# Performance work log

Measured on AMD Instinct MI355X. Metric: run time of the kernel, lower is better.

## Reference

```python
import jax, jax.numpy as jnp
import numpy as np

B, T, N = 4, 512, 16
D, H = 256, 8
CTS, CN, CE = 6, 4, 3
TSE, AUXE = 192, 64  # TSE + AUXE == D
DK = D // H


def pe_table(L, d):
    # sinusoidal positional encoding (annotated-transformer style)
    pos = jnp.arange(L, dtype=jnp.float32)[:, None]
    div = jnp.exp(jnp.arange(0, d, 2, dtype=jnp.float32) * (-jnp.log(jnp.float32(10000.0)) / d))
    pe = jnp.zeros((L, d), dtype=jnp.float32)
    pe = pe.at[:, 0::2].set(jnp.sin(pos * div)).at[:, 1::2].set(jnp.cos(pos * div))
    return pe


def setup_inputs() -> dict:
    key = jax.random.key(0)
    ks = jax.random.split(key, 32)
    s = 0.02
    inp = {
        'x': jax.random.normal(ks[0], (B, T, D), jnp.float32),
        'masked_data': jax.random.normal(ks[1], (B, N, CTS, T), jnp.float32),
        'node_aux': jax.random.normal(ks[2], (B, N, CN, T), jnp.float32),
        'edge_aux': jax.random.normal(ks[3], (B, N, CE, T), jnp.float32),
        'attention_mask': jax.random.randint(ks[4], (B, T, N * T), 0, 2, jnp.int32),
        # ts branch
        'W_ts1': jax.random.normal(ks[5], (CTS, TSE)) * s, 'b_ts1': jnp.zeros((TSE,)),
        'W_ts2': jax.random.normal(ks[6], (TSE, TSE)) * s, 'b_ts2': jnp.zeros((TSE,)),
        # node aux branch
        'W_a1': jax.random.normal(ks[7], (CN, AUXE)) * s, 'b_a1': jnp.zeros((AUXE,)),
        'W_a2': jax.random.normal(ks[8], (AUXE, AUXE)) * s, 'b_a2': jnp.zeros((AUXE,)),
        # edge branch
        'W_e1': jax.random.normal(ks[9], (CE, D)) * s, 'b_e1': jnp.zeros((D,)),
        'W_e2': jax.random.normal(ks[10], (D, D)) * s, 'b_e2': jnp.zeros((D,)),
        # multi-head cross-attention
        'Wq': jax.random.normal(ks[11], (D, D)) * s, 'bq': jnp.zeros((D,)),
        'Wk': jax.random.normal(ks[12], (D, D)) * s, 'bk': jnp.zeros((D,)),
        'Wv': jax.random.normal(ks[13], (D, D)) * s, 'bv': jnp.zeros((D,)),
        'Wo': jax.random.normal(ks[14], (D, D)) * s, 'bo': jnp.zeros((D,)),
        # sublayer layernorm
        'ln_g': jnp.ones((D,)), 'ln_b': jnp.zeros((D,)),
    }
    return inp


def reference(x, masked_data, node_aux, edge_aux, attention_mask,
              W_ts1, b_ts1, W_ts2, b_ts2, W_a1, b_a1, W_a2, b_a2,
              W_e1, b_e1, W_e2, b_e2, Wq, bq, Wk, bk, Wv, bv, Wo, bo,
              ln_g, ln_b):
    pe = pe_table(T, D)  # [T, D]
    xq = x + pe[None]  # pe applied to query sequence (dropout=identity in eval)

    # per-neighbor ts MLP: transpose [B,N,C,T] -> [B,N,T,C], two Linears with ReLU between
    ts = jax.nn.relu(jnp.einsum('bnct,ce->bnte', masked_data, W_ts1) + b_ts1)
    ts = ts @ W_ts2 + b_ts2  # [B,N,T,TSE]
    aux = jax.nn.relu(jnp.einsum('bnct,ce->bnte', node_aux, W_a1) + b_a1)
    aux = aux @ W_a2 + b_a2  # [B,N,T,AUXE]
    nbr = jnp.concatenate([ts, aux], axis=-1)  # [B,N,T,D]

    edge = jax.nn.relu(jnp.einsum('bnct,cd->bntd', edge_aux, W_e1) + b_e1)
    edge = edge @ W_e2 + b_e2  # [B,N,T,D]

    # PE applied per neighbor (positions restart each neighbor), then concat over kv seq
    keys = (nbr * edge + pe[None, None]).reshape(B, N * T, D)
    vals = (nbr + pe[None, None]).reshape(B, N * T, D)

    # SublayerConnection: xq + attn(LayerNorm(xq), keys, vals, mask)
    mu = xq.mean(-1, keepdims=True)
    var = ((xq - mu) ** 2).mean(-1, keepdims=True)
    xn = (xq - mu) / jnp.sqrt(var + 1e-6) * ln_g + ln_b

    q = (xn @ Wq + bq).reshape(B, T, H, DK).transpose(0, 2, 1, 3)        # [B,H,T,DK]
    k = (keys @ Wk + bk).reshape(B, N * T, H, DK).transpose(0, 2, 1, 3)  # [B,H,NT,DK]
    v = (vals @ Wv + bv).reshape(B, N * T, H, DK).transpose(0, 2, 1, 3)

    scores = jnp.einsum('bhqd,bhkd->bhqk', q, k) / jnp.sqrt(jnp.float32(DK))
    scores = jnp.where(attention_mask[:, None, :, :] == 0, jnp.float32(-1e9), scores)
    attn = jax.nn.softmax(scores, axis=-1)
    ctx = jnp.einsum('bhqk,bhkd->bhqd', attn, v).transpose(0, 2, 1, 3).reshape(B, T, D)
    out = ctx @ Wo + bo
    return xq + out
```

## Files before the change

kernel.cpp:

```cpp
#include <hip/hip_runtime.h>
#include <hip/hip_bf16.h>

#define B_ 4
#define T_ 512
#define N_ 16
#define D_ 256
#define H_ 8
#define DK_ 32
#define NT_ (N_ * T_)
#define CTS_ 6
#define CN_ 4
#define CE_ 3
#define TSE_ 192
#define AUXE_ 64
#define SPLIT_ 8
#define KWORDS_ (NT_ / 64)

#define QSCALE_ 0.2550689747f

#define HTS_S 204
#define HAUX_S 76
#define HED_S 268
#define SK_S 268

typedef unsigned long long ull;
typedef unsigned int uint;
typedef __bf16 bf16x8 __attribute__((ext_vector_type(8)));
typedef float f32x4 __attribute__((ext_vector_type(4)));
typedef float f32x16 __attribute__((ext_vector_type(16)));

__global__ __launch_bounds__(256) void pe_kernel(float* pe) {
    int t = blockIdx.x;
    int d = threadIdx.x;
    int j = d >> 1;
    float div = expf((float)(2 * j) * (-9.210340371976184f / 256.0f));
    float a = (float)t * div;
    pe[t * D_ + d] = (d & 1) ? cosf(a) : sinf(a);
}

__global__ __launch_bounds__(256) void maskbits_kernel(const int* __restrict__ mask,
                                                       ull* __restrict__ bitsT) {
    int row = blockIdx.x;
    int b = row >> 9, t = row & (T_ - 1);
    const int* mrow = mask + (size_t)row * NT_;
    int lane = threadIdx.x & 63, wave = threadIdx.x >> 6;
    for (int it = 0; it < NT_ / 256; ++it) {
        int k = it * 256 + wave * 64 + lane;
        ull bal = __ballot(mrow[k] != 0);
        if (lane == 0) bitsT[((size_t)b * KWORDS_ + (k >> 6)) * T_ + t] = bal;
    }
}

__global__ __launch_bounds__(256) void wprep_kernel(
    const float* __restrict__ W_ts1, const float* __restrict__ W_a1,
    const float* __restrict__ W_e1, const float* __restrict__ W_ts2,
    const float* __restrict__ W_a2, const float* __restrict__ W_e2,
    const float* __restrict__ Wk, const float* __restrict__ Wv,
    const float* __restrict__ Wq, const float* __restrict__ Wo,
    __bf16* __restrict__ ts1P, __bf16* __restrict__ a1P, __bf16* __restrict__ e1P,
    __bf16* __restrict__ ts2T, __bf16* __restrict__ a2T, __bf16* __restrict__ e2T,
    __bf16* __restrict__ WkT, __bf16* __restrict__ WvT,
    __bf16* __restrict__ WqT, __bf16* __restrict__ WoT) {
    int i = blockIdx.x * 256 + threadIdx.x;
    if (i < 6144) { int col = i >> 5, k = i & 31;
        ts1P[i] = (__bf16)(k < 6 ? W_ts1[k * TSE_ + col] : 0.f); return; }
    i -= 6144;
    if (i < 2048) { int col = i >> 5, k = i & 31;
        a1P[i] = (__bf16)((k >= 6 && k < 10) ? W_a1[(k - 6) * AUXE_ + col] : 0.f); return; }
    i -= 2048;
    if (i < 8192) { int col = i >> 5, k = i & 31;
        e1P[i] = (__bf16)((k >= 10 && k < 13) ? W_e1[(k - 10) * D_ + col] : 0.f); return; }
    i -= 8192;
    if (i < 36864) {
        int tile = i >> 9, lr = (i >> 5) & 15, kk = i & 31;
        int ct = tile / 6, ks = tile % 6;
        ts2T[i] = (__bf16)W_ts2[(ks * 32 + kk) * TSE_ + ct * 16 + lr]; return; }
    i -= 36864;
    if (i < 4096) {
        int tile = i >> 9, lr = (i >> 5) & 15, kk = i & 31;
        int ct = tile / 2, ks = tile % 2;
        a2T[i] = (__bf16)W_a2[(ks * 32 + kk) * AUXE_ + ct * 16 + lr]; return; }
    i -= 4096;
    if (i < 65536) {
        int tile = i >> 9, lr = (i >> 5) & 15, kk = i & 31;
        int ct = tile >> 3, ks = tile & 7;
        e2T[i] = (__bf16)W_e2[(ks * 32 + kk) * D_ + ct * 16 + lr]; return; }
    i -= 65536;
    if (i < 65536) {
        int tile = i >> 9, lr = (i >> 5) & 15, kk = i & 31;
        int ct = tile >> 3, ks = tile & 7;
        WkT[i] = (__bf16)Wk[(ks * 32 + kk) * D_ + ct * 16 + lr]; return; }
    i -= 65536;
    if (i < 65536) {
        int tile = i >> 9, lr = (i >> 5) & 15, kk = i & 31;
        int ct = tile >> 3, ks = tile & 7;
        WvT[i] = (__bf16)Wv[(ks * 32 + kk) * D_ + ct * 16 + lr]; return; }
    i -= 65536;
    if (i < 65536) {
        int tile = i >> 9, lr = (i >> 5) & 15, kk = i & 31;
        int ct = tile >> 3, ks = tile & 7;
        WqT[i] = (__bf16)(Wq[(ks * 32 + kk) * D_ + ct * 16 + lr] * QSCALE_); return; }
    i -= 65536;
    {
        int tile = i >> 9, lr = (i >> 5) & 15, kk = i & 31;
        int ct = tile >> 3, ks = tile & 7;
        WoT[i] = (__bf16)Wo[(ks * 32 + kk) * D_ + ct * 16 + lr]; }
}

__global__ __launch_bounds__(256, 4) void kv_mfma_kernel(
    const float* __restrict__ md, const float* __restrict__ na, const float* __restrict__ ea,
    const __bf16* __restrict__ ts1P, const __bf16* __restrict__ a1P,
    const __bf16* __restrict__ e1P,
    const float* __restrict__ b_ts1, const float* __restrict__ b_a1,
    const float* __restrict__ b_e1,
    const __bf16* __restrict__ ts2T, const __bf16* __restrict__ a2T,
    const __bf16* __restrict__ e2T,
    const float* __restrict__ b_ts2, const float* __restrict__ b_a2,
    const float* __restrict__ b_e2,
    const __bf16* __restrict__ WkT, const float* __restrict__ bk,
    const __bf16* __restrict__ WvT, const float* __restrict__ bv,
    const float* __restrict__ pe, __bf16* __restrict__ Kb, __bf16* __restrict__ Vf) {
    int blk = blockIdx.x;
    int t0 = (blk & 15) * 32;
    int n = (blk >> 4) & 15;
    int b = blk >> 8;
    int tid = threadIdx.x, lane = tid & 63;
    int wq = tid >> 6;
    int lr = lane & 15, lg = lane >> 4;

    __shared__ __bf16 sA[32 * 40];
    __shared__ __bf16 sU[17536];
    __bf16* hts = sU;
    __bf16* haux = sU + 6528;
    __bf16* hedge = sU + 8960;
    __bf16* skey = sU;
    __bf16* sval = sU + 8576;

    for (int i = tid; i < 32 * 40; i += 256) sA[i] = (__bf16)0.f;
    __syncthreads();
    {
        int t = tid & 31, c0 = tid >> 5;
        size_t bn = (size_t)b * N_ + n;
        for (int c = c0; c < 13; c += 8) {
            float v;
            if (c < 6) v = md[(bn * CTS_ + c) * T_ + t0 + t];
            else if (c < 10) v = na[(bn * CN_ + (c - 6)) * T_ + t0 + t];
            else v = ea[(bn * CE_ + (c - 10)) * T_ + t0 + t];
            sA[t * 40 + c] = (__bf16)v;
        }
    }
    __syncthreads();

    int foff = lr * 32 + lg * 8;
    f32x4 z4 = {0.f, 0.f, 0.f, 0.f};
    bf16x8 a1f0 = *(const bf16x8*)(sA + lr * 40 + lg * 8);
    bf16x8 a1f1 = *(const bf16x8*)(sA + (16 + lr) * 40 + lg * 8);
    int crow0 = lg * 4;

    {
        bool isTs = (wq < 3);
#pragma unroll
        for (int i = 0; i < 4; ++i) {
            int ctn = wq * 4 + i;
            const __bf16* src = isTs ? (ts1P + ctn * 512) : (a1P + (ctn - 12) * 512);
            bf16x8 bf = *(const bf16x8*)(src + foff);
            f32x4 c0 = __builtin_amdgcn_mfma_f32_16x16x32_bf16(a1f0, bf, z4, 0, 0, 0);
            f32x4 c1 = __builtin_amdgcn_mfma_f32_16x16x32_bf16(a1f1, bf, z4, 0, 0, 0);
            if (isTs) {
                int gcol = ctn * 16 + lr;
                float bias = b_ts1[gcol];
#pragma unroll
                for (int r = 0; r < 4; ++r) {
                    hts[(crow0 + r) * HTS_S + gcol] = (__bf16)fmaxf(c0[r] + bias, 0.f);
                    hts[(16 + crow0 + r) * HTS_S + gcol] = (__bf16)fmaxf(c1[r] + bias, 0.f);
                }
            } else {
                int acol = (ctn - 12) * 16 + lr;
                float bias = b_a1[acol];
#pragma unroll
                for (int r = 0; r < 4; ++r) {
                    haux[(crow0 + r) * HAUX_S + acol] = (__bf16)fmaxf(c0[r] + bias, 0.f);
                    haux[(16 + crow0 + r) * HAUX_S + acol] = (__bf16)fmaxf(c1[r] + bias, 0.f);
                }
            }
        }
#pragma unroll
        for (int i = 0; i < 4; ++i) {
            int cte = wq * 4 + i;
            bf16x8 bf = *(const bf16x8*)(e1P + cte * 512 + foff);
            f32x4 c0 = __builtin_amdgcn_mfma_f32_16x16x32_bf16(a1f0, bf, z4, 0, 0, 0);
            f32x4 c1 = __builtin_amdgcn_mfma_f32_16x16x32_bf16(a1f1, bf, z4, 0, 0, 0);
            int gcol = cte * 16 + lr;
            float bias = b_e1[gcol];
#pragma unroll
            for (int r = 0; r < 4; ++r) {
                hedge[(crow0 + r) * HED_S + gcol] = (__bf16)fmaxf(c0[r] + bias, 0.f);
                hedge[(16 + crow0 + r) * HED_S + gcol] = (__bf16)fmaxf(c1[r] + bias, 0.f);
            }
        }
    }
    __syncthreads();

    f32x4 eacc[2][4];
#pragma unroll
    for (int i = 0; i < 4; ++i) { eacc[0][i] = z4; eacc[1][i] = z4; }
    {
        const __bf16* ebase = e2T + (size_t)(wq * 4) * 8 * 512 + foff;
        bf16x8 bcur[4];
#pragma unroll
        for (int i = 0; i < 4; ++i) bcur[i] = *(const bf16x8*)(ebase + i * 4096);
#pragma unroll 1
        for (int ks = 0; ks < 8; ++ks) {
            bf16x8 bnext[4];
            if (ks < 7) {
#pragma unroll
                for (int i = 0; i < 4; ++i)
                    bnext[i] = *(const bf16x8*)(ebase + i * 4096 + (ks + 1) * 512);
            }
            __builtin_amdgcn_sched_barrier(0);
            bf16x8 af0 = *(const bf16x8*)(hedge + lr * HED_S + ks * 32 + lg * 8);
            bf16x8 af1 = *(const bf16x8*)(hedge + (16 + lr) * HED_S + ks * 32 + lg * 8);
#pragma unroll
            for (int i = 0; i < 4; ++i) {
                eacc[0][i] = __builtin_amdgcn_mfma_f32_16x16x32_bf16(af0, bcur[i], eacc[0][i], 0, 0, 0);
                eacc[1][i] = __builtin_amdgcn_mfma_f32_16x16x32_bf16(af1, bcur[i], eacc[1][i], 0, 0, 0);
            }
            if (ks < 7) {
#pragma unroll
                for (int i = 0; i < 4; ++i) bcur[i] = bnext[i];
            }
        }
    }

    f32x4 nacc[2][4];
#pragma unroll
    for (int i = 0; i < 4; ++i) { nacc[0][i] = z4; nacc[1][i] = z4; }
    if (wq < 3) {
        const __bf16* nbase = ts2T + (size_t)(wq * 4) * 6 * 512 + foff;
        bf16x8 bcur[4];
#pragma unroll
        for (int i = 0; i < 4; ++i) bcur[i] = *(const bf16x8*)(nbase + i * 3072);
#pragma unroll 1
        for (int ks = 0; ks < 6; ++ks) {
            bf16x8 bnext[4];
            if (ks < 5) {
#pragma unroll
                for (int i = 0; i < 4; ++i)
                    bnext[i] = *(const bf16x8*)(nbase + i * 3072 + (ks + 1) * 512);
            }
            __builtin_amdgcn_sched_barrier(0);
            bf16x8 af0 = *(const bf16x8*)(hts + lr * HTS_S + ks * 32 + lg * 8);
            bf16x8 af1 = *(const bf16x8*)(hts + (16 + lr) * HTS_S + ks * 32 + lg * 8);
#pragma unroll
            for (int i = 0; i < 4; ++i) {
                nacc[0][i] = __builtin_amdgcn_mfma_f32_16x16x32_bf16(af0, bcur[i], nacc[0][i], 0, 0, 0);
                nacc[1][i] = __builtin_amdgcn_mfma_f32_16x16x32_bf16(af1, bcur[i], nacc[1][i], 0, 0, 0);
            }
            if (ks < 5) {
#pragma unroll
                for (int i = 0; i < 4; ++i) bcur[i] = bnext[i];
            }
        }
    } else {
#pragma unroll
        for (int ks = 0; ks < 2; ++ks) {
            bf16x8 af0 = *(const bf16x8*)(haux + lr * HAUX_S + ks * 32 + lg * 8);
            bf16x8 af1 = *(const bf16x8*)(haux + (16 + lr) * HAUX_S + ks * 32 + lg * 8);
#pragma unroll
            for (int i = 0; i < 4; ++i) {
                bf16x8 bf = *(const bf16x8*)(a2T + (i * 2 + ks) * 512 + foff);
                nacc[0][i] = __builtin_amdgcn_mfma_f32_16x16x32_bf16(af0, bf, nacc[0][i], 0, 0, 0);
                nacc[1][i] = __builtin_amdgcn_mfma_f32_16x16x32_bf16(af1, bf, nacc[1][i], 0, 0, 0);
            }
        }
    }
    __syncthreads();

#pragma unroll
    for (int i = 0; i < 4; ++i) {
        int gcol = wq * 64 + i * 16 + lr;
        float nb_bias = (wq < 3) ? b_ts2[gcol] : b_a2[gcol - 192];
        float ed_bias = b_e2[gcol];
#pragma unroll
        for (int rf = 0; rf < 2; ++rf)
#pragma unroll
            for (int r = 0; r < 4; ++r) {
                int row = rf * 16 + crow0 + r;
                float p = pe[(t0 + row) * D_ + gcol];
                float nb = nacc[rf][i][r] + nb_bias;
                float ed = eacc[rf][i][r] + ed_bias;
                skey[row * SK_S + gcol] = (__bf16)(nb * ed + p);
                sval[row * SK_S + gcol] = (__bf16)(nb + p);
            }
    }
    __syncthreads();

    size_t key0 = (size_t)n * T_ + t0;

    {
        const __bf16* kbse = WkT + (size_t)(wq * 4) * 8 * 512 + foff;
        f32x4 ka[2][4];
#pragma unroll
        for (int i = 0; i < 4; ++i) { ka[0][i] = z4; ka[1][i] = z4; }
        bf16x8 bcur[4];
#pragma unroll
        for (int i = 0; i < 4; ++i) bcur[i] = *(const bf16x8*)(kbse + i * 4096);
#pragma unroll 1
        for (int ks = 0; ks < 8; ++ks) {
            bf16x8 bnext[4];
            if (ks < 7) {
#pragma unroll
                for (int i = 0; i < 4; ++i)
                    bnext[i] = *(const bf16x8*)(kbse + i * 4096 + (ks + 1) * 512);
            }
            __builtin_amdgcn_sched_barrier(0);
            bf16x8 af0 = *(const bf16x8*)(skey + lr * SK_S + ks * 32 + lg * 8);
            bf16x8 af1 = *(const bf16x8*)(skey + (16 + lr) * SK_S + ks * 32 + lg * 8);
#pragma unroll
            for (int i = 0; i < 4; ++i) {
                ka[0][i] = __builtin_amdgcn_mfma_f32_16x16x32_bf16(af0, bcur[i], ka[0][i], 0, 0, 0);
                ka[1][i] = __builtin_amdgcn_mfma_f32_16x16x32_bf16(af1, bcur[i], ka[1][i], 0, 0, 0);
            }
            if (ks < 7) {
#pragma unroll
                for (int i = 0; i < 4; ++i) bcur[i] = bnext[i];
            }
        }
#pragma unroll
        for (int i = 0; i < 4; ++i) {
            int gcol = wq * 64 + i * 16 + lr;
            float kbias = bk[gcol];
            int h = gcol >> 5, dd = gcol & 31;
            size_t bh = (size_t)b * H_ + h;
#pragma unroll
            for (int rf = 0; rf < 2; ++rf) {
                int crow = rf * 16 + crow0;
#pragma unroll
                for (int r = 0; r < 4; ++r)
                    Kb[(bh * NT_ + key0 + crow + r) * DK_ + dd] = (__bf16)(ka[rf][i][r] + kbias);
            }
        }
    }

    {
        const __bf16* vbse = WvT + (size_t)(wq * 4) * 8 * 512 + foff;
        f32x4 va[2][4];
#pragma unroll
        for (int i = 0; i < 4; ++i) { va[0][i] = z4; va[1][i] = z4; }
        bf16x8 bcur[4];
#pragma unroll
        for (int i = 0; i < 4; ++i) bcur[i] = *(const bf16x8*)(vbse + i * 4096);
#pragma unroll 1
        for (int ks = 0; ks < 8; ++ks) {
            bf16x8 bnext[4];
            if (ks < 7) {
#pragma unroll
                for (int i = 0; i < 4; ++i)
                    bnext[i] = *(const bf16x8*)(vbse + i * 4096 + (ks + 1) * 512);
            }
            __builtin_amdgcn_sched_barrier(0);
            bf16x8 af0 = *(const bf16x8*)(sval + lr * SK_S + ks * 32 + lg * 8);
            bf16x8 af1 = *(const bf16x8*)(sval + (16 + lr) * SK_S + ks * 32 + lg * 8);
#pragma unroll
            for (int i = 0; i < 4; ++i) {
                va[0][i] = __builtin_amdgcn_mfma_f32_16x16x32_bf16(af0, bcur[i], va[0][i], 0, 0, 0);
                va[1][i] = __builtin_amdgcn_mfma_f32_16x16x32_bf16(af1, bcur[i], va[1][i], 0, 0, 0);
            }
            if (ks < 7) {
#pragma unroll
                for (int i = 0; i < 4; ++i) bcur[i] = bnext[i];
            }
        }
#pragma unroll
        for (int i = 0; i < 4; ++i) {
            int gcol = wq * 64 + i * 16 + lr;
            float vbias = bv[gcol];
            int h = gcol >> 5, dd = gcol & 31;
            size_t bh = (size_t)b * H_ + h;
#pragma unroll
            for (int rf = 0; rf < 2; ++rf) {
                int crow = rf * 16 + crow0;
                __bf16 tmp[4];
#pragma unroll
                for (int r = 0; r < 4; ++r) tmp[r] = (__bf16)(va[rf][i][r] + vbias);
                size_t kg = key0 + crow;
                int within = (int)(kg & 63);
                int vks = within >> 4, vl5 = (within >> 3) & 1, j0 = within & 7;
                size_t tile = kg >> 6;
                size_t vaddr = ((bh * (NT_ / 64) + tile) * 4 + vks) * 512 +
                               (size_t)(vl5 * 32 + dd) * 8 + j0;
                *(ushort4*)(Vf + vaddr) = *(ushort4*)tmp;
            }
        }
    }
}

__global__ __launch_bounds__(256) void q_mfma_kernel(
    const float* __restrict__ x, const float* __restrict__ pe,
    const __bf16* __restrict__ WqT, const float* __restrict__ bq,
    const float* __restrict__ ln_g, const float* __restrict__ ln_b,
    __bf16* __restrict__ Qb) {
    int blk = blockIdx.x;
    int t0 = (blk & 15) * 32;
    int b = blk >> 4;
    int tid = threadIdx.x, lane = tid & 63;
    int wq = tid >> 6, lr = lane & 15, lg = lane >> 4;

    __shared__ __bf16 s_xn[32 * SK_S];

    {
        int row = tid >> 3, sub = tid & 7;
        size_t roff = ((size_t)b * T_ + t0 + row) * D_;
        const float* pr = pe + (t0 + row) * D_;
        f32x4 vv[8];
        float s1 = 0.f, s2 = 0.f;
#pragma unroll
        for (int q4 = 0; q4 < 8; ++q4) {
            int c = q4 * 32 + sub * 4;
            f32x4 xv = *(const f32x4*)(x + roff + c);
            f32x4 pv = *(const f32x4*)(pr + c);
            f32x4 t4;
#pragma unroll
            for (int j = 0; j < 4; ++j) {
                t4[j] = xv[j] + pv[j];
                s1 += t4[j];
                s2 += t4[j] * t4[j];
            }
            vv[q4] = t4;
        }
#pragma unroll
        for (int o = 1; o <= 4; o <<= 1) {
            s1 += __shfl_xor(s1, o, 64);
            s2 += __shfl_xor(s2, o, 64);
        }
        float mu = s1 * (1.f / D_);
        float var = s2 * (1.f / D_) - mu * mu;
        float rs = rsqrtf(var + 1e-6f);
#pragma unroll
        for (int q4 = 0; q4 < 8; ++q4) {
            int c = q4 * 32 + sub * 4;
            f32x4 g4 = *(const f32x4*)(ln_g + c);
            f32x4 b4 = *(const f32x4*)(ln_b + c);
#pragma unroll
            for (int j = 0; j < 4; ++j)
                s_xn[row * SK_S + c + j] = (__bf16)((vv[q4][j] - mu) * rs * g4[j] + b4[j]);
        }
    }
    __syncthreads();

    int foff = lr * 32 + lg * 8;
    int crow0 = lg * 4;
    f32x4 z4 = {0.f, 0.f, 0.f, 0.f};
    f32x4 qa[2][4];
#pragma unroll
    for (int i = 0; i < 4; ++i) { qa[0][i] = z4; qa[1][i] = z4; }
    const __bf16* qbse = WqT + (size_t)(wq * 4) * 8 * 512 + foff;
#pragma unroll
    for (int ks = 0; ks < 8; ++ks) {
        bf16x8 af0 = *(const bf16x8*)(s_xn + lr * SK_S + ks * 32 + lg * 8);
        bf16x8 af1 = *(const bf16x8*)(s_xn + (16 + lr) * SK_S + ks * 32 + lg * 8);
#pragma unroll
        for (int i = 0; i < 4; ++i) {
            bf16x8 b8 = *(const bf16x8*)(qbse + i * 4096 + ks * 512);
            qa[0][i] = __builtin_amdgcn_mfma_f32_16x16x32_bf16(af0, b8, qa[0][i], 0, 0, 0);
            qa[1][i] = __builtin_amdgcn_mfma_f32_16x16x32_bf16(af1, b8, qa[1][i], 0, 0, 0);
        }
    }
#pragma unroll
    for (int i = 0; i < 4; ++i) {
        int gcol = wq * 64 + i * 16 + lr;
        float bias = bq[gcol] * QSCALE_;
#pragma unroll
        for (int rf = 0; rf < 2; ++rf)
#pragma unroll
            for (int r = 0; r < 4; ++r)
                Qb[((size_t)b * T_ + t0 + rf * 16 + crow0 + r) * D_ + gcol] =
                    (__bf16)(qa[rf][i][r] + bias);
    }
}

__global__ __launch_bounds__(256, 4) void attn_mfma_kernel(
    const __bf16* __restrict__ Qb, const __bf16* __restrict__ Kb,
    const __bf16* __restrict__ Vf, const ull* __restrict__ bitsT,
    float* __restrict__ Opart, float* __restrict__ Lpart) {
    int blk = blockIdx.x;
    int kh = blk & (SPLIT_ - 1);
    int qt = (blk >> 3) & 3;
    int h = (blk >> 5) & 7;
    int b = blk >> 8;
    int tid = threadIdx.x, lane = tid & 63, w = tid >> 6;
    int lq = lane & 31, l5 = lane >> 5;

    const size_t bh = (size_t)b * H_ + h;
    const int TILES = KWORDS_ / SPLIT_;

    int qglob = qt * 128 + w * 32 + lq;
    const __bf16* qbase = Qb + ((size_t)b * T_ + qglob) * D_ + h * DK_ + l5 * 8;
    bf16x8 qf0 = *(const bf16x8*)(qbase);
    bf16x8 qf1 = *(const bf16x8*)(qbase + 16);

    const __bf16* kp = Kb + bh * NT_ * DK_ + (size_t)(kh * TILES) * 64 * DK_;
    const __bf16* vp = Vf + (bh * (NT_ / 64) + (size_t)(kh * TILES)) * 2048;
    const ull* mp = bitsT + (size_t)b * KWORDS_ * T_ + (size_t)(kh * TILES) * T_ + qglob;

    int k00 = lq * DK_ + l5 * 8;
    int k01 = k00 + 16;
    int k10 = (32 + lq) * DK_ + l5 * 8;
    int k11 = k10 + 16;
    int shamt = 4 * l5;

    f32x16 acc, acc_l, zv;
#pragma unroll
    for (int i = 0; i < 16; ++i) { acc[i] = 0.f; acc_l[i] = 0.f; zv[i] = 0.f; }
    union { uint u[4]; bf16x8 v; } onesf;
    onesf.u[0] = 0x3F803F80u; onesf.u[1] = 0x3F803F80u;
    onesf.u[2] = 0x3F803F80u; onesf.u[3] = 0x3F803F80u;

    bf16x8 kc0 = *(const bf16x8*)(kp + k00);
    bf16x8 kc1 = *(const bf16x8*)(kp + k01);
    bf16x8 kc2 = *(const bf16x8*)(kp + k10);
    bf16x8 kc3 = *(const bf16x8*)(kp + k11);
    ull mw = *mp;

#pragma unroll 1
    for (int kt = 0; kt < TILES; ++kt) {
        bf16x8 vc0 = *(const bf16x8*)(vp + 0 * 512 + lane * 8);
        bf16x8 vc1 = *(const bf16x8*)(vp + 1 * 512 + lane * 8);
        bf16x8 vc2 = *(const bf16x8*)(vp + 2 * 512 + lane * 8);
        bf16x8 vc3 = *(const bf16x8*)(vp + 3 * 512 + lane * 8);
        bf16x8 kn0, kn1, kn2, kn3;
        ull mn = 0;
        if (kt + 1 < TILES) {
            kn0 = *(const bf16x8*)(kp + 2048 + k00);
            kn1 = *(const bf16x8*)(kp + 2048 + k01);
            kn2 = *(const bf16x8*)(kp + 2048 + k10);
            kn3 = *(const bf16x8*)(kp + 2048 + k11);
            mn = mp[T_];
        }
        __builtin_amdgcn_sched_barrier(0);

        ull sh = mw >> shamt;

#pragma unroll
        for (int s = 0; s < 2; ++s) {
            f32x16 sc = __builtin_amdgcn_mfma_f32_32x32x16_bf16(
                s ? kc2 : kc0, qf0, zv, 0, 0, 0);
            sc = __builtin_amdgcn_mfma_f32_32x32x16_bf16(
                s ? kc3 : kc1, qf1, sc, 0, 0, 0);

            uint ms = (uint)(sh >> (32 * s));
            float p[16];
#pragma unroll
            for (int r = 0; r < 16; ++r) {
                int pos = (r & 3) + 8 * (r >> 2);
                float e = __builtin_amdgcn_exp2f(sc[r]);
                int mb = __builtin_amdgcn_sbfe((int)ms, (uint)pos, 1u);
                p[r] = __uint_as_float(__float_as_uint(e) & (uint)mb);
            }

#pragma unroll
            for (int h2 = 0; h2 < 2; ++h2) {
                uint w0, w1, w2, w3;
                asm("v_cvt_pk_bf16_f32 %0, %1, %2" : "=v"(w0) : "v"(p[8 * h2 + 0]), "v"(p[8 * h2 + 1]));
                asm("v_cvt_pk_bf16_f32 %0, %1, %2" : "=v"(w1) : "v"(p[8 * h2 + 2]), "v"(p[8 * h2 + 3]));
                asm("v_cvt_pk_bf16_f32 %0, %1, %2" : "=v"(w2) : "v"(p[8 * h2 + 4]), "v"(p[8 * h2 + 5]));
                asm("v_cvt_pk_bf16_f32 %0, %1, %2" : "=v"(w3) : "v"(p[8 * h2 + 6]), "v"(p[8 * h2 + 7]));
                asm volatile("v_permlane32_swap_b32 %0, %1" : "+v"(w0), "+v"(w2));
                asm volatile("v_permlane32_swap_b32 %0, %1" : "+v"(w1), "+v"(w3));
                union { uint u[4]; bf16x8 v; } pa;
                pa.u[0] = w0; pa.u[1] = w1; pa.u[2] = w2; pa.u[3] = w3;
                bf16x8 vfr = (s == 0) ? (h2 == 0 ? vc0 : vc1) : (h2 == 0 ? vc2 : vc3);
                acc = __builtin_amdgcn_mfma_f32_32x32x16_bf16(pa.v, vfr, acc, 0, 0, 0);
                acc_l = __builtin_amdgcn_mfma_f32_32x32x16_bf16(pa.v, onesf.v, acc_l, 0, 0, 0);
            }
        }

        kp += 2048;
        vp += 2048;
        mp += T_;
        if (kt + 1 < TILES) {
            kc0 = kn0; kc1 = kn1; kc2 = kn2; kc3 = kn3;
            mw = mn;
        }
    }

    size_t obase = (((size_t)kh * B_ + b) * H_ + h) * T_ + qt * 128 + w * 32;
#pragma unroll
    for (int r = 0; r < 16; ++r) {
        int q = (r & 3) + 8 * (r >> 2) + 4 * l5;
        Opart[(obase + q) * DK_ + lq] = acc[r];
    }
    if (lq == 0) {
#pragma unroll
        for (int r = 0; r < 16; ++r) {
            int q = (r & 3) + 8 * (r >> 2) + 4 * l5;
            Lpart[obase + q] = acc_l[r];
        }
    }
}

__global__ __launch_bounds__(256) void merge_kernel(
    const float* __restrict__ Opart, const float* __restrict__ Lpart,
    __bf16* __restrict__ ctxb) {
    int idx = blockIdx.x * 256 + threadIdx.x;
    int d = idx & 31;
    int t = (idx >> 5) & (T_ - 1);
    int bh = idx >> 14;
    int h = bh & 7, b = bh >> 3;
    size_t ps = (size_t)B_ * H_ * T_;
    size_t base = (size_t)bh * T_ + t;
    float L = 0.f, o = 0.f;
#pragma unroll
    for (int s = 0; s < SPLIT_; ++s) {
        L += Lpart[s * ps + base];
        o += Opart[(s * ps + base) * DK_ + d];
    }
    ctxb[((size_t)b * T_ + t) * D_ + h * DK_ + d] = (__bf16)(o / L);
}

__global__ __launch_bounds__(256) void out_mfma_kernel(
    const __bf16* __restrict__ ctxb, const float* __restrict__ x,
    const float* __restrict__ pe, const __bf16* __restrict__ WoT,
    const float* __restrict__ bo, float* __restrict__ out) {
    int blk = blockIdx.x;
    int t0 = (blk & 15) * 32;
    int b = blk >> 4;
    int tid = threadIdx.x, lane = tid & 63;
    int wq = tid >> 6, lr = lane & 15, lg = lane >> 4;

    __shared__ __bf16 sc_[32 * SK_S];
    for (int idx = tid; idx < 32 * 64; idx += 256) {
        int r = idx >> 6, c4 = (idx & 63) * 4;
        *(ushort4*)(sc_ + r * SK_S + c4) =
            *(const ushort4*)(ctxb + ((size_t)b * T_ + t0 + r) * D_ + c4);
    }
    __syncthreads();

    int foff = lr * 32 + lg * 8;
    int crow0 = lg * 4;
    f32x4 z4 = {0.f, 0.f, 0.f, 0.f};
    f32x4 oa[2][4];
#pragma unroll
    for (int i = 0; i < 4; ++i) { oa[0][i] = z4; oa[1][i] = z4; }
    const __bf16* obse = WoT + (size_t)(wq * 4) * 8 * 512 + foff;
#pragma unroll
    for (int ks = 0; ks < 8; ++ks) {
        bf16x8 af0 = *(const bf16x8*)(sc_ + lr * SK_S + ks * 32 + lg * 8);
        bf16x8 af1 = *(const bf16x8*)(sc_ + (16 + lr) * SK_S + ks * 32 + lg * 8);
#pragma unroll
        for (int i = 0; i < 4; ++i) {
            bf16x8 b8 = *(const bf16x8*)(obse + i * 4096 + ks * 512);
            oa[0][i] = __builtin_amdgcn_mfma_f32_16x16x32_bf16(af0, b8, oa[0][i], 0, 0, 0);
            oa[1][i] = __builtin_amdgcn_mfma_f32_16x16x32_bf16(af1, b8, oa[1][i], 0, 0, 0);
        }
    }
#pragma unroll
    for (int i = 0; i < 4; ++i) {
        int gcol = wq * 64 + i * 16 + lr;
        float bias = bo[gcol];
#pragma unroll
        for (int rf = 0; rf < 2; ++rf)
#pragma unroll
            for (int r = 0; r < 4; ++r) {
                int t = t0 + rf * 16 + crow0 + r;
                size_t off = ((size_t)b * T_ + t) * D_ + gcol;
                out[off] = x[off] + pe[t * D_ + gcol] + oa[rf][i][r] + bias;
            }
    }
}

extern "C" void kernel_launch(void* const* d_in, const int* in_sizes, int n_in,
                              void* d_out, int out_size, void* d_ws, size_t ws_size,
                              hipStream_t stream) {
    const float* x = (const float*)d_in[0];
    const float* md = (const float*)d_in[1];
    const float* na = (const float*)d_in[2];
    const float* ea = (const float*)d_in[3];
    const int* mask = (const int*)d_in[4];
    const float* W_ts1 = (const float*)d_in[5];
    const float* b_ts1 = (const float*)d_in[6];
    const float* W_ts2 = (const float*)d_in[7];
    const float* b_ts2 = (const float*)d_in[8];
    const float* W_a1 = (const float*)d_in[9];
    const float* b_a1 = (const float*)d_in[10];
    const float* W_a2 = (const float*)d_in[11];
    const float* b_a2 = (const float*)d_in[12];
    const float* W_e1 = (const float*)d_in[13];
    const float* b_e1 = (const float*)d_in[14];
    const float* W_e2 = (const float*)d_in[15];
    const float* b_e2 = (const float*)d_in[16];
    const float* Wq = (const float*)d_in[17];
    const float* bq = (const float*)d_in[18];
    const float* Wk = (const float*)d_in[19];
    const float* bk = (const float*)d_in[20];
    const float* Wv = (const float*)d_in[21];
    const float* bv = (const float*)d_in[22];
    const float* Wo = (const float*)d_in[23];
    const float* bo = (const float*)d_in[24];
    const float* ln_g = (const float*)d_in[25];
    const float* ln_b = (const float*)d_in[26];
    float* out = (float*)d_out;

    char* ws = (char*)d_ws;
    float* pe = (float*)ws;     ws += (size_t)T_ * D_ * 4;
    ull* bitsT = (ull*)ws;      ws += (size_t)B_ * KWORDS_ * T_ * 8;
    __bf16* Kb = (__bf16*)ws;   ws += (size_t)B_ * H_ * NT_ * DK_ * 2;
    __bf16* Vf = (__bf16*)ws;   ws += (size_t)B_ * H_ * NT_ * DK_ * 2;
    __bf16* Qb = (__bf16*)ws;   ws += (size_t)B_ * T_ * D_ * 2;
    __bf16* ctxb = (__bf16*)ws; ws += (size_t)B_ * T_ * D_ * 2;
    float* Opart = (float*)ws;  ws += (size_t)SPLIT_ * B_ * H_ * T_ * DK_ * 4;
    float* Lpart = (float*)ws;  ws += (size_t)SPLIT_ * B_ * H_ * T_ * 4;
    __bf16* ts1P = (__bf16*)ws; ws += 6144 * 2;
    __bf16* a1P = (__bf16*)ws;  ws += 2048 * 2;
    __bf16* e1P = (__bf16*)ws;  ws += 8192 * 2;
    __bf16* ts2T = (__bf16*)ws; ws += 36864 * 2;
    __bf16* a2T = (__bf16*)ws;  ws += 4096 * 2;
    __bf16* e2T = (__bf16*)ws;  ws += 65536 * 2;
    __bf16* WkT = (__bf16*)ws;  ws += 65536 * 2;
    __bf16* WvT = (__bf16*)ws;  ws += 65536 * 2;
    __bf16* WqT = (__bf16*)ws;  ws += 65536 * 2;
    __bf16* WoT = (__bf16*)ws;  ws += 65536 * 2;

    pe_kernel<<<T_, 256, 0, stream>>>(pe);
    maskbits_kernel<<<B_ * T_, 256, 0, stream>>>(mask, bitsT);
    wprep_kernel<<<1504, 256, 0, stream>>>(W_ts1, W_a1, W_e1, W_ts2, W_a2, W_e2,
                                           Wk, Wv, Wq, Wo,
                                           ts1P, a1P, e1P, ts2T, a2T, e2T,
                                           WkT, WvT, WqT, WoT);
    kv_mfma_kernel<<<B_ * N_ * (T_ / 32), 256, 0, stream>>>(
        md, na, ea, ts1P, a1P, e1P, b_ts1, b_a1, b_e1,
        ts2T, a2T, e2T, b_ts2, b_a2, b_e2, WkT, bk, WvT, bv, pe, Kb, Vf);
    q_mfma_kernel<<<B_ * (T_ / 32), 256, 0, stream>>>(x, pe, WqT, bq, ln_g, ln_b, Qb);
    attn_mfma_kernel<<<B_ * H_ * (T_ / 128) * SPLIT_, 256, 0, stream>>>(
        Qb, Kb, Vf, bitsT, Opart, Lpart);
    merge_kernel<<<(B_ * H_ * T_ * DK_) / 256, 256, 0, stream>>>(Opart, Lpart, ctxb);
    out_mfma_kernel<<<B_ * (T_ / 32), 256, 0, stream>>>(ctxb, x, pe, WoT, bo, out);
}
```

Measured before the change: 123.6 us.

## Fuse split-K merge into output projection and double attention split count

Removes the separate merge kernel: the output projection kernel now reduces the partial attention outputs and normalizers from all splits directly into shared memory before the Wo GEMM, eliminating the ctx buffer round trip and one launch. The attention split factor is raised from 8 to 16 with a higher occupancy hint, giving twice as many attention blocks for better GPU fill. In exchange, partial buffers double in size and the out kernel, with only 64 blocks, must read 16 partials per element, which may make that stage memory-latency bound.

```diff
diff --git a/kernel.cpp b/kernel.cpp
--- a/kernel.cpp
+++ b/kernel.cpp
@@ -13,7 +13,7 @@
 #define CE_ 3
 #define TSE_ 192
 #define AUXE_ 64
-#define SPLIT_ 8
+#define SPLIT_ 16
 #define KWORDS_ (NT_ / 64)
 
 #define QSCALE_ 0.2550689747f
@@ -479,15 +479,15 @@
     }
 }
 
-__global__ __launch_bounds__(256, 4) void attn_mfma_kernel(
+__global__ __launch_bounds__(256, 8) void attn_mfma_kernel(
     const __bf16* __restrict__ Qb, const __bf16* __restrict__ Kb,
     const __bf16* __restrict__ Vf, const ull* __restrict__ bitsT,
     float* __restrict__ Opart, float* __restrict__ Lpart) {
     int blk = blockIdx.x;
     int kh = blk & (SPLIT_ - 1);
-    int qt = (blk >> 3) & 3;
-    int h = (blk >> 5) & 7;
-    int b = blk >> 8;
+    int qt = (blk >> 4) & 3;
+    int h = (blk >> 6) & 7;
+    int b = blk >> 9;
     int tid = threadIdx.x, lane = tid & 63, w = tid >> 6;
     int lq = lane & 31, l5 = lane >> 5;
 
@@ -599,29 +599,11 @@
     }
 }
 
-__global__ __launch_bounds__(256) void merge_kernel(
+__global__ __launch_bounds__(256) void out_mfma_kernel(
     const float* __restrict__ Opart, const float* __restrict__ Lpart,
-    __bf16* __restrict__ ctxb) {
-    int idx = blockIdx.x * 256 + threadIdx.x;
-    int d = idx & 31;
-    int t = (idx >> 5) & (T_ - 1);
-    int bh = idx >> 14;
-    int h = bh & 7, b = bh >> 3;
-    size_t ps = (size_t)B_ * H_ * T_;
-    size_t base = (size_t)bh * T_ + t;
-    float L = 0.f, o = 0.f;
-#pragma unroll
-    for (int s = 0; s < SPLIT_; ++s) {
-        L += Lpart[s * ps + base];
-        o += Opart[(s * ps + base) * DK_ + d];
-    }
-    ctxb[((size_t)b * T_ + t) * D_ + h * DK_ + d] = (__bf16)(o / L);
-}
-
-__global__ __launch_bounds__(256) void out_mfma_kernel(
-    const __bf16* __restrict__ ctxb, const float* __restrict__ x,
-    const float* __restrict__ pe, const __bf16* __restrict__ WoT,
-    const float* __restrict__ bo, float* __restrict__ out) {
+    const float* __restrict__ x, const float* __restrict__ pe,
+    const __bf16* __restrict__ WoT, const float* __restrict__ bo,
+    float* __restrict__ out) {
     int blk = blockIdx.x;
     int t0 = (blk & 15) * 32;
     int b = blk >> 4;
@@ -629,10 +611,33 @@
     int wq = tid >> 6, lr = lane & 15, lg = lane >> 4;
 
     __shared__ __bf16 sc_[32 * SK_S];
+    __shared__ float sLinv[32 * 8];
+    size_t ps = (size_t)B_ * H_ * T_;
+
+    {
+        int row = tid >> 3, hh = tid & 7;
+        size_t base = ((size_t)b * H_ + hh) * T_ + t0 + row;
+        float L = 0.f;
+#pragma unroll
+        for (int s = 0; s < SPLIT_; ++s) L += Lpart[s * ps + base];
+        sLinv[row * 8 + hh] = 1.0f / L;
+    }
+    __syncthreads();
+
     for (int idx = tid; idx < 32 * 64; idx += 256) {
-        int r = idx >> 6, c4 = (idx & 63) * 4;
-        *(ushort4*)(sc_ + r * SK_S + c4) =
-            *(const ushort4*)(ctxb + ((size_t)b * T_ + t0 + r) * D_ + c4);
+        int r = idx >> 6, g = idx & 63;
+        int hh = g >> 3, d4 = (g & 7) * 4;
+        size_t base = (((size_t)b * H_ + hh) * T_ + t0 + r) * DK_ + d4;
+        f32x4 o = {0.f, 0.f, 0.f, 0.f};
+#pragma unroll
+        for (int s = 0; s < SPLIT_; ++s) {
+            f32x4 t4 = *(const f32x4*)(Opart + s * ps * DK_ + base);
+            o[0] += t4[0]; o[1] += t4[1]; o[2] += t4[2]; o[3] += t4[3];
+        }
+        float li = sLinv[r * 8 + hh];
+        int c = hh * 32 + d4;
+#pragma unroll
+        for (int j = 0; j < 4; ++j) sc_[r * SK_S + c + j] = (__bf16)(o[j] * li);
     }
     __syncthreads();
 
@@ -707,7 +712,6 @@
     __bf16* Kb = (__bf16*)ws;   ws += (size_t)B_ * H_ * NT_ * DK_ * 2;
     __bf16* Vf = (__bf16*)ws;   ws += (size_t)B_ * H_ * NT_ * DK_ * 2;
     __bf16* Qb = (__bf16*)ws;   ws += (size_t)B_ * T_ * D_ * 2;
-    __bf16* ctxb = (__bf16*)ws; ws += (size_t)B_ * T_ * D_ * 2;
     float* Opart = (float*)ws;  ws += (size_t)SPLIT_ * B_ * H_ * T_ * DK_ * 4;
     float* Lpart = (float*)ws;  ws += (size_t)SPLIT_ * B_ * H_ * T_ * 4;
     __bf16* ts1P = (__bf16*)ws; ws += 6144 * 2;
@@ -733,6 +737,5 @@
     q_mfma_kernel<<<B_ * (T_ / 32), 256, 0, stream>>>(x, pe, WqT, bq, ln_g, ln_b, Qb);
     attn_mfma_kernel<<<B_ * H_ * (T_ / 128) * SPLIT_, 256, 0, stream>>>(
         Qb, Kb, Vf, bitsT, Opart, Lpart);
-    merge_kernel<<<(B_ * H_ * T_ * DK_) / 256, 256, 0, stream>>>(Opart, Lpart, ctxb);
-    out_mfma_kernel<<<B_ * (T_ / 32), 256, 0, stream>>>(ctxb, x, pe, WoT, bo, out);
+    out_mfma_kernel<<<B_ * (T_ / 32), 256, 0, stream>>>(Opart, Lpart, x, pe, WoT, bo, out);
 }
```

After: 453.9 us. 3.67x slower.
